# Performance work log

Measured on AMD Instinct MI355X. Metric: run time of the kernel, lower is better.

Reference implementation:

```python
import jax, jax.numpy as jnp
import numpy as np


def setup_inputs() -> dict:
    key = jax.random.key(0)
    kq, kk, kv = jax.random.split(key, 3)
    B, Hq, Hkv, S, D = 2, 16, 4, 2048, 64
    q = jax.random.normal(kq, (B, Hq, S, D), dtype=jnp.float32)
    k = jax.random.normal(kk, (B, Hkv, S, D), dtype=jnp.float32)
    v = jax.random.normal(kv, (B, Hkv, S, D), dtype=jnp.float32)
    return {"q": q, "k": k, "v": v}


def reference(q, k, v):
    # SDPA MATH backend: softmax(q k^T * scale) v, with GQA head repetition.
    Hq = q.shape[1]
    Hkv = k.shape[1]
    rep = Hq // Hkv
    if rep > 1:
        k = jnp.repeat(k, rep, axis=1)  # [B,Hq,S,D]
        v = jnp.repeat(v, rep, axis=1)
    scale = 1.0 / jnp.sqrt(jnp.asarray(q.shape[-1], dtype=q.dtype))
    scores = jnp.einsum("bhqd,bhkd->bhqk", q, k) * scale  # [B,Hq,S,S]
    attn = jax.nn.softmax(scores, axis=-1)
    return jnp.einsum("bhqk,bhkd->bhqd", attn, v)
```

## Files before the change

kernel.cpp:

```cpp
#include <hip/hip_runtime.h>
#include <hip/hip_bf16.h>

typedef unsigned short u16;
typedef short s16x4 __attribute__((ext_vector_type(4)));
typedef short s16x8 __attribute__((ext_vector_type(8)));
typedef float fx4 __attribute__((ext_vector_type(4)));
typedef unsigned ux2 __attribute__((ext_vector_type(2)));

#define BATCH 2
#define NHQ 16
#define NHKV 4
#define SEQ 2048
#define HD 64
#define TM 128
#define TN 128
#define NTILES (SEQ / TN)
#define VSTRIDE 132
#define NKV (BATCH * NHKV * SEQ * HD)
#define QSCALE 0.18033688011112042f

__device__ __forceinline__ unsigned pack2_bf16(float a, float b) {
    const unsigned ua = __float_as_uint(a) + 0x8000u;
    const unsigned ub = __float_as_uint(b) + 0x8000u;
    return __builtin_amdgcn_perm(ub, ua, 0x07060302u);
}
__device__ __forceinline__ unsigned ilv_lo(unsigned r0, unsigned r1) {
    return __builtin_amdgcn_perm(r1, r0, 0x05040100u);
}
__device__ __forceinline__ unsigned ilv_hi(unsigned r0, unsigned r1) {
    return __builtin_amdgcn_perm(r1, r0, 0x07060302u);
}

__global__ __launch_bounds__(256) void cvt_kv_kernel(
    const float* __restrict__ K, const float* __restrict__ V,
    u16* __restrict__ wsK, u16* __restrict__ wsV)
{
    const int i = (blockIdx.x * 256 + threadIdx.x) * 4;
    const fx4 k4 = *(const fx4*)(K + i);
    const fx4 v4 = *(const fx4*)(V + i);
    ux2 ko, vo;
    ko[0] = pack2_bf16(k4[0], k4[1]);
    ko[1] = pack2_bf16(k4[2], k4[3]);
    vo[0] = pack2_bf16(v4[0], v4[1]);
    vo[1] = pack2_bf16(v4[2], v4[3]);
    *(ux2*)(wsK + i) = ko;
    *(ux2*)(wsV + i) = vo;
}

__global__ __launch_bounds__(256, 2) void ptSDPA_39668317946373_kernel(
    const float* __restrict__ gQ,
    const u16* __restrict__ wsK,
    const u16* __restrict__ wsV,
    float* __restrict__ gO)
{
    __shared__ u16 shK[2][TN * HD];
    __shared__ u16 shVt[2][HD * VSTRIDE];

    const int tid = threadIdx.x;
    const int wv  = tid >> 6;
    const int ln  = tid & 63;
    const int l15 = ln & 15;
    const int qd  = ln >> 4;

    const int g     = blockIdx.x;
    const int kvg   = g & 7;
    const int inner = g >> 3;
    const int qtb   = inner & 15;
    const int hqw   = inner >> 4;
    const int batch = kvg >> 2;
    const int hkv   = kvg & 3;
    const int head  = batch * NHQ + hkv * 4 + hqw;

    const int t0 = (inner & 3) * 4;

    const float* q_base = gQ + (size_t)head * SEQ * HD;
    const u16*   k_base = wsK + (size_t)kvg * SEQ * HD;
    const u16*   v_base = wsV + (size_t)kvg * SEQ * HD;
    float*       o_base = gO + (size_t)head * SEQ * HD;

    const int qrow0 = qtb * TM;

    s16x8 qfrag[2][2];
#pragma unroll
    for (int mi = 0; mi < 2; mi++) {
        const int row = qrow0 + wv * 32 + mi * 16 + l15;
#pragma unroll
        for (int ks = 0; ks < 2; ks++) {
            const int d0 = ks * 32 + qd * 8;
            const fx4 lo = *(const fx4*)(q_base + (size_t)row * HD + d0);
            const fx4 hi = *(const fx4*)(q_base + (size_t)row * HD + d0 + 4);
            union { unsigned u[4]; s16x8 v; } t;
            t.u[0] = pack2_bf16(lo[0] * QSCALE, lo[1] * QSCALE);
            t.u[1] = pack2_bf16(lo[2] * QSCALE, lo[3] * QSCALE);
            t.u[2] = pack2_bf16(hi[0] * QSCALE, hi[1] * QSCALE);
            t.u[3] = pack2_bf16(hi[2] * QSCALE, hi[3] * QSCALE);
            qfrag[mi][ks] = t.v;
        }
    }

    fx4 oacc[2][4];
    fx4 racc[2];
    const fx4 z4 = {0.f, 0.f, 0.f, 0.f};
#pragma unroll
    for (int mi = 0; mi < 2; mi++) {
        racc[mi] = z4;
#pragma unroll
        for (int ni = 0; ni < 4; ni++) oacc[mi][ni] = z4;
    }
    const s16x4 ones4 = {(short)0x3F80, (short)0x3F80,
                         (short)0x3F80, (short)0x3F80};

    const int skey  = tid & 127;
    const int shalf = tid >> 7;
    const u16* kp0 = k_base + skey * HD + shalf * 32;
    const int vkey = ln * 2;
    const int vd0  = wv * 16;
    const u16* vp0 = v_base + vkey * HD + vd0;

    s16x8 kreg[4], vreg[4];

#pragma unroll
    for (int s = 0; s < 4; s++)
        kreg[s] = *(const s16x8*)(kp0 + (size_t)t0 * TN * HD + s * 8);
    {
        const u16* vp = vp0 + (size_t)t0 * TN * HD;
        vreg[0] = *(const s16x8*)(vp);
        vreg[1] = *(const s16x8*)(vp + 8);
        vreg[2] = *(const s16x8*)(vp + HD);
        vreg[3] = *(const s16x8*)(vp + HD + 8);
    }
#pragma unroll
    for (int s = 0; s < 4; s++) {
        const int c = shalf * 4 + s;
        *(s16x8*)(shK[0] + skey * 64 + ((c ^ (skey & 7)) * 8)) = kreg[s];
    }
#pragma unroll
    for (int h = 0; h < 2; h++) {
        union { s16x8 v; unsigned u[4]; } r0, r1;
        r0.v = vreg[h];
        r1.v = vreg[2 + h];
#pragma unroll
        for (int c2 = 0; c2 < 4; c2++) {
            const int d = vd0 + h * 8 + c2 * 2;
            *(unsigned*)(shVt[0] + d * VSTRIDE + vkey) = ilv_lo(r0.u[c2], r1.u[c2]);
            *(unsigned*)(shVt[0] + (d + 1) * VSTRIDE + vkey) = ilv_hi(r0.u[c2], r1.u[c2]);
        }
    }

#pragma unroll 2
    for (int i = 0; i < NTILES; i++) {
        const int cur = i & 1;
        const int nxt = cur ^ 1;

        __syncthreads();

        if (i + 1 < NTILES) {
            const int tp = (t0 + i + 1) & (NTILES - 1);
            const u16* kp = kp0 + (size_t)tp * TN * HD;
            const u16* vp = vp0 + (size_t)tp * TN * HD;
#pragma unroll
            for (int s = 0; s < 4; s++) kreg[s] = *(const s16x8*)(kp + s * 8);
            vreg[0] = *(const s16x8*)(vp);
            vreg[1] = *(const s16x8*)(vp + 8);
            vreg[2] = *(const s16x8*)(vp + HD);
            vreg[3] = *(const s16x8*)(vp + HD + 8);
        }

        const int kb7 = l15 & 7;
        const int sw0 = (qd ^ kb7) << 3;
        const int sw1 = ((4 + qd) ^ kb7) << 3;
        const u16* kRow = shK[cur] + l15 * 64;

        fx4 scp[2][2];
        {
            const s16x8 kf0 = *(const s16x8*)(kRow + sw0);
            const s16x8 kf1 = *(const s16x8*)(kRow + sw1);
#pragma unroll
            for (int mi = 0; mi < 2; mi++)
                scp[0][mi] = __builtin_amdgcn_mfma_f32_16x16x32_bf16(
                    kf0, qfrag[mi][0], z4, 0, 0, 0);
#pragma unroll
            for (int mi = 0; mi < 2; mi++)
                scp[0][mi] = __builtin_amdgcn_mfma_f32_16x16x32_bf16(
                    kf1, qfrag[mi][1], scp[0][mi], 0, 0, 0);
        }

#pragma unroll
        for (int kt = 0; kt < 8; kt++) {
            const int p = kt & 1;
            if (kt < 7) {
                const s16x8 kf0 = *(const s16x8*)(kRow + (kt + 1) * 1024 + sw0);
                const s16x8 kf1 = *(const s16x8*)(kRow + (kt + 1) * 1024 + sw1);
#pragma unroll
                for (int mi = 0; mi < 2; mi++)
                    scp[p ^ 1][mi] = __builtin_amdgcn_mfma_f32_16x16x32_bf16(
                        kf0, qfrag[mi][0], z4, 0, 0, 0);
#pragma unroll
                for (int mi = 0; mi < 2; mi++)
                    scp[p ^ 1][mi] = __builtin_amdgcn_mfma_f32_16x16x32_bf16(
                        kf1, qfrag[mi][1], scp[p ^ 1][mi], 0, 0, 0);
            }

            const int kb = kt * 16 + qd * 4;
            s16x4 vf[4];
#pragma unroll
            for (int ni = 0; ni < 4; ni++)
                vf[ni] = *(const s16x4*)(
                    shVt[cur] + (ni * 16 + l15) * VSTRIDE + kb);

            s16x4 pf[2];
#pragma unroll
            for (int mi = 0; mi < 2; mi++) {
                const float p0 = __builtin_amdgcn_exp2f(scp[p][mi][0]);
                const float p1 = __builtin_amdgcn_exp2f(scp[p][mi][1]);
                const float p2 = __builtin_amdgcn_exp2f(scp[p][mi][2]);
                const float p3 = __builtin_amdgcn_exp2f(scp[p][mi][3]);
                union { unsigned u[2]; s16x4 v; } pp;
                pp.u[0] = pack2_bf16(p0, p1);
                pp.u[1] = pack2_bf16(p2, p3);
                pf[mi] = pp.v;
            }

#pragma unroll
            for (int mi = 0; mi < 2; mi++)
                racc[mi] = __builtin_amdgcn_mfma_f32_16x16x16bf16_1k(
                    pf[mi], ones4, racc[mi], 0, 0, 0);

#pragma unroll
            for (int ni = 0; ni < 4; ni++) {
#pragma unroll
                for (int mi = 0; mi < 2; mi++)
                    oacc[mi][ni] = __builtin_amdgcn_mfma_f32_16x16x16bf16_1k(
                        pf[mi], vf[ni], oacc[mi][ni], 0, 0, 0);
            }
        }

        if (i + 1 < NTILES) {
#pragma unroll
            for (int s = 0; s < 4; s++) {
                const int c = shalf * 4 + s;
                *(s16x8*)(shK[nxt] + skey * 64 + ((c ^ (skey & 7)) * 8)) = kreg[s];
            }
#pragma unroll
            for (int h = 0; h < 2; h++) {
                union { s16x8 v; unsigned u[4]; } r0, r1;
                r0.v = vreg[h];
                r1.v = vreg[2 + h];
#pragma unroll
                for (int c2 = 0; c2 < 4; c2++) {
                    const int d = vd0 + h * 8 + c2 * 2;
                    *(unsigned*)(shVt[nxt] + d * VSTRIDE + vkey) =
                        ilv_lo(r0.u[c2], r1.u[c2]);
                    *(unsigned*)(shVt[nxt] + (d + 1) * VSTRIDE + vkey) =
                        ilv_hi(r0.u[c2], r1.u[c2]);
                }
            }
        }
    }

#pragma unroll
    for (int mi = 0; mi < 2; mi++) {
        float inv[4];
#pragma unroll
        for (int r = 0; r < 4; r++) inv[r] = 1.0f / racc[mi][r];
#pragma unroll
        for (int ni = 0; ni < 4; ni++)
#pragma unroll
            for (int r = 0; r < 4; r++) {
                const int qr = qrow0 + wv * 32 + mi * 16 + qd * 4 + r;
                o_base[(size_t)qr * HD + ni * 16 + l15] =
                    oacc[mi][ni][r] * inv[r];
            }
    }
}

extern "C" void kernel_launch(void* const* d_in, const int* in_sizes, int n_in,
                              void* d_out, int out_size, void* d_ws, size_t ws_size,
                              hipStream_t stream) {
    const float* q = (const float*)d_in[0];
    const float* k = (const float*)d_in[1];
    const float* v = (const float*)d_in[2];
    float*       o = (float*)d_out;
    u16* wsK = (u16*)d_ws;
    u16* wsV = wsK + NKV;
    cvt_kv_kernel<<<NKV / 1024, 256, 0, stream>>>(k, v, wsK, wsV);
    const dim3 grid(BATCH * NHQ * (SEQ / TM));
    ptSDPA_39668317946373_kernel<<<grid, 256, 0, stream>>>(q, wsK, wsV, o);
}
```

Baseline: 126.3 us.

## Use 8 waves per block with 16 query rows each and split K/V loading

Doubles the block to 512 threads so each wave owns 16 query rows instead of 32, halving per-wave accumulators and MFMA work per tile. The global-to-LDS staging is split so that half the waves load V (with transpose) and half load K, instead of every thread loading both. The goal is more waves in flight to hide latency, with lower register pressure and less staging work per thread. In exchange each wave does less MFMA work per LDS fragment read, so K/V shared-memory reads per FLOP go up, and there is more barrier overhead across a larger block.

Result: faster. 123.3 us (-2.4%).

```diff
diff --git a/kernel.cpp b/kernel.cpp
--- a/kernel.cpp
+++ b/kernel.cpp
@@ -47,7 +47,7 @@
     *(ux2*)(wsV + i) = vo;
 }
 
-__global__ __launch_bounds__(256, 2) void ptSDPA_39668317946373_kernel(
+__global__ __launch_bounds__(512, 4) void ptSDPA_39668317946373_kernel(
     const float* __restrict__ gQ,
     const u16* __restrict__ wsK,
     const u16* __restrict__ wsV,
@@ -80,10 +80,9 @@
 
     const int qrow0 = qtb * TM;
 
-    s16x8 qfrag[2][2];
-#pragma unroll
-    for (int mi = 0; mi < 2; mi++) {
-        const int row = qrow0 + wv * 32 + mi * 16 + l15;
+    s16x8 qfrag[2];
+    {
+        const int row = qrow0 + wv * 16 + l15;
 #pragma unroll
         for (int ks = 0; ks < 2; ks++) {
             const int d0 = ks * 32 + qd * 8;
@@ -94,56 +93,58 @@
             t.u[1] = pack2_bf16(lo[2] * QSCALE, lo[3] * QSCALE);
             t.u[2] = pack2_bf16(hi[0] * QSCALE, hi[1] * QSCALE);
             t.u[3] = pack2_bf16(hi[2] * QSCALE, hi[3] * QSCALE);
-            qfrag[mi][ks] = t.v;
-        }
-    }
-
-    fx4 oacc[2][4];
-    fx4 racc[2];
+            qfrag[ks] = t.v;
+        }
+    }
+
+    fx4 oacc[4];
+    fx4 racc;
     const fx4 z4 = {0.f, 0.f, 0.f, 0.f};
-#pragma unroll
-    for (int mi = 0; mi < 2; mi++) {
-        racc[mi] = z4;
-#pragma unroll
-        for (int ni = 0; ni < 4; ni++) oacc[mi][ni] = z4;
-    }
+    racc = z4;
+#pragma unroll
+    for (int ni = 0; ni < 4; ni++) oacc[ni] = z4;
     const s16x4 ones4 = {(short)0x3F80, (short)0x3F80,
                          (short)0x3F80, (short)0x3F80};
 
-    const int skey  = tid & 127;
-    const int shalf = tid >> 7;
+    const bool isV = (wv < 4);
+    const int  st  = isV ? tid : (tid - 256);
+    const int vkey = (st & 63) * 2;
+    const int vd0  = (st >> 6) * 16;
+    const u16* vp0 = v_base + vkey * HD + vd0;
+    const int skey  = st & 127;
+    const int shalf = st >> 7;
     const u16* kp0 = k_base + skey * HD + shalf * 32;
-    const int vkey = ln * 2;
-    const int vd0  = wv * 16;
-    const u16* vp0 = v_base + vkey * HD + vd0;
-
-    s16x8 kreg[4], vreg[4];
-
-#pragma unroll
-    for (int s = 0; s < 4; s++)
-        kreg[s] = *(const s16x8*)(kp0 + (size_t)t0 * TN * HD + s * 8);
-    {
+
+    s16x8 preg[4];
+
+    if (isV) {
         const u16* vp = vp0 + (size_t)t0 * TN * HD;
-        vreg[0] = *(const s16x8*)(vp);
-        vreg[1] = *(const s16x8*)(vp + 8);
-        vreg[2] = *(const s16x8*)(vp + HD);
-        vreg[3] = *(const s16x8*)(vp + HD + 8);
-    }
-#pragma unroll
-    for (int s = 0; s < 4; s++) {
-        const int c = shalf * 4 + s;
-        *(s16x8*)(shK[0] + skey * 64 + ((c ^ (skey & 7)) * 8)) = kreg[s];
-    }
-#pragma unroll
-    for (int h = 0; h < 2; h++) {
-        union { s16x8 v; unsigned u[4]; } r0, r1;
-        r0.v = vreg[h];
-        r1.v = vreg[2 + h];
-#pragma unroll
-        for (int c2 = 0; c2 < 4; c2++) {
-            const int d = vd0 + h * 8 + c2 * 2;
-            *(unsigned*)(shVt[0] + d * VSTRIDE + vkey) = ilv_lo(r0.u[c2], r1.u[c2]);
-            *(unsigned*)(shVt[0] + (d + 1) * VSTRIDE + vkey) = ilv_hi(r0.u[c2], r1.u[c2]);
+        preg[0] = *(const s16x8*)(vp);
+        preg[1] = *(const s16x8*)(vp + 8);
+        preg[2] = *(const s16x8*)(vp + HD);
+        preg[3] = *(const s16x8*)(vp + HD + 8);
+#pragma unroll
+        for (int h = 0; h < 2; h++) {
+            union { s16x8 v; unsigned u[4]; } r0, r1;
+            r0.v = preg[h];
+            r1.v = preg[2 + h];
+#pragma unroll
+            for (int c2 = 0; c2 < 4; c2++) {
+                const int d = vd0 + h * 8 + c2 * 2;
+                *(unsigned*)(shVt[0] + d * VSTRIDE + vkey) =
+                    ilv_lo(r0.u[c2], r1.u[c2]);
+                *(unsigned*)(shVt[0] + (d + 1) * VSTRIDE + vkey) =
+                    ilv_hi(r0.u[c2], r1.u[c2]);
+            }
+        }
+    } else {
+#pragma unroll
+        for (int s = 0; s < 4; s++)
+            preg[s] = *(const s16x8*)(kp0 + (size_t)t0 * TN * HD + s * 8);
+#pragma unroll
+        for (int s = 0; s < 4; s++) {
+            const int c = shalf * 4 + s;
+            *(s16x8*)(shK[0] + skey * 64 + ((c ^ (skey & 7)) * 8)) = preg[s];
         }
     }
 
@@ -156,14 +157,18 @@
 
         if (i + 1 < NTILES) {
             const int tp = (t0 + i + 1) & (NTILES - 1);
-            const u16* kp = kp0 + (size_t)tp * TN * HD;
-            const u16* vp = vp0 + (size_t)tp * TN * HD;
-#pragma unroll
-            for (int s = 0; s < 4; s++) kreg[s] = *(const s16x8*)(kp + s * 8);
-            vreg[0] = *(const s16x8*)(vp);
-            vreg[1] = *(const s16x8*)(vp + 8);
-            vreg[2] = *(const s16x8*)(vp + HD);
-            vreg[3] = *(const s16x8*)(vp + HD + 8);
+            if (isV) {
+                const u16* vp = vp0 + (size_t)tp * TN * HD;
+                preg[0] = *(const s16x8*)(vp);
+                preg[1] = *(const s16x8*)(vp + 8);
+                preg[2] = *(const s16x8*)(vp + HD);
+                preg[3] = *(const s16x8*)(vp + HD + 8);
+            } else {
+                const u16* kp = kp0 + (size_t)tp * TN * HD;
+#pragma unroll
+                for (int s = 0; s < 4; s++)
+                    preg[s] = *(const s16x8*)(kp + s * 8);
+            }
         }
 
         const int kb7 = l15 & 7;
@@ -171,18 +176,14 @@
         const int sw1 = ((4 + qd) ^ kb7) << 3;
         const u16* kRow = shK[cur] + l15 * 64;
 
-        fx4 scp[2][2];
+        fx4 scp[2];
         {
             const s16x8 kf0 = *(const s16x8*)(kRow + sw0);
             const s16x8 kf1 = *(const s16x8*)(kRow + sw1);
-#pragma unroll
-            for (int mi = 0; mi < 2; mi++)
-                scp[0][mi] = __builtin_amdgcn_mfma_f32_16x16x32_bf16(
-                    kf0, qfrag[mi][0], z4, 0, 0, 0);
-#pragma unroll
-            for (int mi = 0; mi < 2; mi++)
-                scp[0][mi] = __builtin_amdgcn_mfma_f32_16x16x32_bf16(
-                    kf1, qfrag[mi][1], scp[0][mi], 0, 0, 0);
+            scp[0] = __builtin_amdgcn_mfma_f32_16x16x32_bf16(
+                kf0, qfrag[0], z4, 0, 0, 0);
+            scp[0] = __builtin_amdgcn_mfma_f32_16x16x32_bf16(
+                kf1, qfrag[1], scp[0], 0, 0, 0);
         }
 
 #pragma unroll
@@ -191,14 +192,10 @@
             if (kt < 7) {
                 const s16x8 kf0 = *(const s16x8*)(kRow + (kt + 1) * 1024 + sw0);
                 const s16x8 kf1 = *(const s16x8*)(kRow + (kt + 1) * 1024 + sw1);
-#pragma unroll
-                for (int mi = 0; mi < 2; mi++)
-                    scp[p ^ 1][mi] = __builtin_amdgcn_mfma_f32_16x16x32_bf16(
-                        kf0, qfrag[mi][0], z4, 0, 0, 0);
-#pragma unroll
-                for (int mi = 0; mi < 2; mi++)
-                    scp[p ^ 1][mi] = __builtin_amdgcn_mfma_f32_16x16x32_bf16(
-                        kf1, qfrag[mi][1], scp[p ^ 1][mi], 0, 0, 0);
+                scp[p ^ 1] = __builtin_amdgcn_mfma_f32_16x16x32_bf16(
+                    kf0, qfrag[0], z4, 0, 0, 0);
+                scp[p ^ 1] = __builtin_amdgcn_mfma_f32_16x16x32_bf16(
+                    kf1, qfrag[1], scp[p ^ 1], 0, 0, 0);
             }
 
             const int kb = kt * 16 + qd * 4;
@@ -208,68 +205,62 @@
                 vf[ni] = *(const s16x4*)(
                     shVt[cur] + (ni * 16 + l15) * VSTRIDE + kb);
 
-            s16x4 pf[2];
-#pragma unroll
-            for (int mi = 0; mi < 2; mi++) {
-                const float p0 = __builtin_amdgcn_exp2f(scp[p][mi][0]);
-                const float p1 = __builtin_amdgcn_exp2f(scp[p][mi][1]);
-                const float p2 = __builtin_amdgcn_exp2f(scp[p][mi][2]);
-                const float p3 = __builtin_amdgcn_exp2f(scp[p][mi][3]);
-                union { unsigned u[2]; s16x4 v; } pp;
-                pp.u[0] = pack2_bf16(p0, p1);
-                pp.u[1] = pack2_bf16(p2, p3);
-                pf[mi] = pp.v;
-            }
-
-#pragma unroll
-            for (int mi = 0; mi < 2; mi++)
-                racc[mi] = __builtin_amdgcn_mfma_f32_16x16x16bf16_1k(
-                    pf[mi], ones4, racc[mi], 0, 0, 0);
-
-#pragma unroll
-            for (int ni = 0; ni < 4; ni++) {
-#pragma unroll
-                for (int mi = 0; mi < 2; mi++)
-                    oacc[mi][ni] = __builtin_amdgcn_mfma_f32_16x16x16bf16_1k(
-                        pf[mi], vf[ni], oacc[mi][ni], 0, 0, 0);
-            }
+            const float p0 = __builtin_amdgcn_exp2f(scp[p][0]);
+            const float p1 = __builtin_amdgcn_exp2f(scp[p][1]);
+            const float p2 = __builtin_amdgcn_exp2f(scp[p][2]);
+            const float p3 = __builtin_amdgcn_exp2f(scp[p][3]);
+            union { unsigned u[2]; s16x4 v; } pp;
+            pp.u[0] = pack2_bf16(p0, p1);
+            pp.u[1] = pack2_bf16(p2, p3);
+            const s16x4 pf = pp.v;
+
+            racc = __builtin_amdgcn_mfma_f32_16x16x16bf16_1k(
+                pf, ones4, racc, 0, 0, 0);
+
+#pragma unroll
+            for (int ni = 0; ni < 4; ni++)
+                oacc[ni] = __builtin_amdgcn_mfma_f32_16x16x16bf16_1k(
+                    pf, vf[ni], oacc[ni], 0, 0, 0);
         }
 
         if (i + 1 < NTILES) {
-#pragma unroll
-            for (int s = 0; s < 4; s++) {
-                const int c = shalf * 4 + s;
-                *(s16x8*)(shK[nxt] + skey * 64 + ((c ^ (skey & 7)) * 8)) = kreg[s];
-            }
-#pragma unroll
-            for (int h = 0; h < 2; h++) {
-                union { s16x8 v; unsigned u[4]; } r0, r1;
-                r0.v = vreg[h];
-                r1.v = vreg[2 + h];
-#pragma unroll
-                for (int c2 = 0; c2 < 4; c2++) {
-                    const int d = vd0 + h * 8 + c2 * 2;
-                    *(unsigned*)(shVt[nxt] + d * VSTRIDE + vkey) =
-                        ilv_lo(r0.u[c2], r1.u[c2]);
-                    *(unsigned*)(shVt[nxt] + (d + 1) * VSTRIDE + vkey) =
-                        ilv_hi(r0.u[c2], r1.u[c2]);
+            if (isV) {
+#pragma unroll
+                for (int h = 0; h < 2; h++) {
+                    union { s16x8 v; unsigned u[4]; } r0, r1;
+                    r0.v = preg[h];
+                    r1.v = preg[2 + h];
+#pragma unroll
+                    for (int c2 = 0; c2 < 4; c2++) {
+                        const int d = vd0 + h * 8 + c2 * 2;
+                        *(unsigned*)(shVt[nxt] + d * VSTRIDE + vkey) =
+                            ilv_lo(r0.u[c2], r1.u[c2]);
+                        *(unsigned*)(shVt[nxt] + (d + 1) * VSTRIDE + vkey) =
+                            ilv_hi(r0.u[c2], r1.u[c2]);
+                    }
                 }
-            }
-        }
-    }
-
-#pragma unroll
-    for (int mi = 0; mi < 2; mi++) {
+            } else {
+#pragma unroll
+                for (int s = 0; s < 4; s++) {
+                    const int c = shalf * 4 + s;
+                    *(s16x8*)(shK[nxt] + skey * 64 + ((c ^ (skey & 7)) * 8)) =
+                        preg[s];
+                }
+            }
+        }
+    }
+
+    {
         float inv[4];
 #pragma unroll
-        for (int r = 0; r < 4; r++) inv[r] = 1.0f / racc[mi][r];
+        for (int r = 0; r < 4; r++) inv[r] = 1.0f / racc[r];
 #pragma unroll
         for (int ni = 0; ni < 4; ni++)
 #pragma unroll
             for (int r = 0; r < 4; r++) {
-                const int qr = qrow0 + wv * 32 + mi * 16 + qd * 4 + r;
+                const int qr = qrow0 + wv * 16 + qd * 4 + r;
                 o_base[(size_t)qr * HD + ni * 16 + l15] =
-                    oacc[mi][ni][r] * inv[r];
+                    oacc[ni][r] * inv[r];
             }
     }
 }
@@ -285,5 +276,5 @@
     u16* wsV = wsK + NKV;
     cvt_kv_kernel<<<NKV / 1024, 256, 0, stream>>>(k, v, wsK, wsV);
     const dim3 grid(BATCH * NHQ * (SEQ / TM));
-    ptSDPA_39668317946373_kernel<<<grid, 256, 0, stream>>>(q, wsK, wsV, o);
-}
+    ptSDPA_39668317946373_kernel<<<grid, 512, 0, stream>>>(q, wsK, wsV, o);
+}
```

## Split key tile across two wave groups with 512-thread blocks and LDS reduction

Applied to the files above, without the earlier changes.

Doubles the block to 512 threads. Each group of four waves handles half of the 128-key tile for the same 32 query rows, and the two groups' partial output and row-sum accumulators are combined through shared memory at the end. Tile loading is split so the first 256 threads stage V and the other 256 stage K, which halves each thread's prefetch registers. The aim is more waves per CU and more latency hiding. The cost is an extra reduction pass through LDS with two more barriers, and 512-thread blocks that must fit four per CU under the tighter register limit.

Measured after the change: 135.9 us. 7.6% more time.

```diff
diff --git a/kernel.cpp b/kernel.cpp
--- a/kernel.cpp
+++ b/kernel.cpp
@@ -47,7 +47,7 @@
     *(ux2*)(wsV + i) = vo;
 }
 
-__global__ __launch_bounds__(256, 2) void ptSDPA_39668317946373_kernel(
+__global__ __launch_bounds__(512, 4) void ptSDPA_39668317946373_kernel(
     const float* __restrict__ gQ,
     const u16* __restrict__ wsK,
     const u16* __restrict__ wsV,
@@ -58,6 +58,8 @@
 
     const int tid = threadIdx.x;
     const int wv  = tid >> 6;
+    const int qw  = wv & 3;
+    const int kh  = wv >> 2;
     const int ln  = tid & 63;
     const int l15 = ln & 15;
     const int qd  = ln >> 4;
@@ -83,7 +85,7 @@
     s16x8 qfrag[2][2];
 #pragma unroll
     for (int mi = 0; mi < 2; mi++) {
-        const int row = qrow0 + wv * 32 + mi * 16 + l15;
+        const int row = qrow0 + qw * 32 + mi * 16 + l15;
 #pragma unroll
         for (int ks = 0; ks < 2; ks++) {
             const int d0 = ks * 32 + qd * 8;
@@ -110,42 +112,49 @@
     const s16x4 ones4 = {(short)0x3F80, (short)0x3F80,
                          (short)0x3F80, (short)0x3F80};
 
-    const int skey  = tid & 127;
-    const int shalf = tid >> 7;
+    const bool isV = (wv < 4);
+    const int  st  = isV ? tid : (tid - 256);
+    const int vkey = (st & 63) * 2;
+    const int vd0  = (st >> 6) * 16;
+    const u16* vp0 = v_base + vkey * HD + vd0;
+    const int skey  = st & 127;
+    const int shalf = st >> 7;
     const u16* kp0 = k_base + skey * HD + shalf * 32;
-    const int vkey = ln * 2;
-    const int vd0  = wv * 16;
-    const u16* vp0 = v_base + vkey * HD + vd0;
-
-    s16x8 kreg[4], vreg[4];
-
-#pragma unroll
-    for (int s = 0; s < 4; s++)
-        kreg[s] = *(const s16x8*)(kp0 + (size_t)t0 * TN * HD + s * 8);
-    {
+
+    s16x8 preg[4];
+
+    if (isV) {
         const u16* vp = vp0 + (size_t)t0 * TN * HD;
-        vreg[0] = *(const s16x8*)(vp);
-        vreg[1] = *(const s16x8*)(vp + 8);
-        vreg[2] = *(const s16x8*)(vp + HD);
-        vreg[3] = *(const s16x8*)(vp + HD + 8);
-    }
-#pragma unroll
-    for (int s = 0; s < 4; s++) {
-        const int c = shalf * 4 + s;
-        *(s16x8*)(shK[0] + skey * 64 + ((c ^ (skey & 7)) * 8)) = kreg[s];
-    }
-#pragma unroll
-    for (int h = 0; h < 2; h++) {
-        union { s16x8 v; unsigned u[4]; } r0, r1;
-        r0.v = vreg[h];
-        r1.v = vreg[2 + h];
-#pragma unroll
-        for (int c2 = 0; c2 < 4; c2++) {
-            const int d = vd0 + h * 8 + c2 * 2;
-            *(unsigned*)(shVt[0] + d * VSTRIDE + vkey) = ilv_lo(r0.u[c2], r1.u[c2]);
-            *(unsigned*)(shVt[0] + (d + 1) * VSTRIDE + vkey) = ilv_hi(r0.u[c2], r1.u[c2]);
-        }
-    }
+        preg[0] = *(const s16x8*)(vp);
+        preg[1] = *(const s16x8*)(vp + 8);
+        preg[2] = *(const s16x8*)(vp + HD);
+        preg[3] = *(const s16x8*)(vp + HD + 8);
+#pragma unroll
+        for (int h = 0; h < 2; h++) {
+            union { s16x8 v; unsigned u[4]; } r0, r1;
+            r0.v = preg[h];
+            r1.v = preg[2 + h];
+#pragma unroll
+            for (int c2 = 0; c2 < 4; c2++) {
+                const int d = vd0 + h * 8 + c2 * 2;
+                *(unsigned*)(shVt[0] + d * VSTRIDE + vkey) =
+                    ilv_lo(r0.u[c2], r1.u[c2]);
+                *(unsigned*)(shVt[0] + (d + 1) * VSTRIDE + vkey) =
+                    ilv_hi(r0.u[c2], r1.u[c2]);
+            }
+        }
+    } else {
+#pragma unroll
+        for (int s = 0; s < 4; s++)
+            preg[s] = *(const s16x8*)(kp0 + (size_t)t0 * TN * HD + s * 8);
+#pragma unroll
+        for (int s = 0; s < 4; s++) {
+            const int c = shalf * 4 + s;
+            *(s16x8*)(shK[0] + skey * 64 + ((c ^ (skey & 7)) * 8)) = preg[s];
+        }
+    }
+
+    const int ktbase = kh * 4;
 
 #pragma unroll 2
     for (int i = 0; i < NTILES; i++) {
@@ -156,14 +165,18 @@
 
         if (i + 1 < NTILES) {
             const int tp = (t0 + i + 1) & (NTILES - 1);
-            const u16* kp = kp0 + (size_t)tp * TN * HD;
-            const u16* vp = vp0 + (size_t)tp * TN * HD;
-#pragma unroll
-            for (int s = 0; s < 4; s++) kreg[s] = *(const s16x8*)(kp + s * 8);
-            vreg[0] = *(const s16x8*)(vp);
-            vreg[1] = *(const s16x8*)(vp + 8);
-            vreg[2] = *(const s16x8*)(vp + HD);
-            vreg[3] = *(const s16x8*)(vp + HD + 8);
+            if (isV) {
+                const u16* vp = vp0 + (size_t)tp * TN * HD;
+                preg[0] = *(const s16x8*)(vp);
+                preg[1] = *(const s16x8*)(vp + 8);
+                preg[2] = *(const s16x8*)(vp + HD);
+                preg[3] = *(const s16x8*)(vp + HD + 8);
+            } else {
+                const u16* kp = kp0 + (size_t)tp * TN * HD;
+#pragma unroll
+                for (int s = 0; s < 4; s++)
+                    preg[s] = *(const s16x8*)(kp + s * 8);
+            }
         }
 
         const int kb7 = l15 & 7;
@@ -173,8 +186,8 @@
 
         fx4 scp[2][2];
         {
-            const s16x8 kf0 = *(const s16x8*)(kRow + sw0);
-            const s16x8 kf1 = *(const s16x8*)(kRow + sw1);
+            const s16x8 kf0 = *(const s16x8*)(kRow + ktbase * 1024 + sw0);
+            const s16x8 kf1 = *(const s16x8*)(kRow + ktbase * 1024 + sw1);
 #pragma unroll
             for (int mi = 0; mi < 2; mi++)
                 scp[0][mi] = __builtin_amdgcn_mfma_f32_16x16x32_bf16(
@@ -186,11 +199,13 @@
         }
 
 #pragma unroll
-        for (int kt = 0; kt < 8; kt++) {
+        for (int kt = 0; kt < 4; kt++) {
             const int p = kt & 1;
-            if (kt < 7) {
-                const s16x8 kf0 = *(const s16x8*)(kRow + (kt + 1) * 1024 + sw0);
-                const s16x8 kf1 = *(const s16x8*)(kRow + (kt + 1) * 1024 + sw1);
+            if (kt < 3) {
+                const s16x8 kf0 =
+                    *(const s16x8*)(kRow + (ktbase + kt + 1) * 1024 + sw0);
+                const s16x8 kf1 =
+                    *(const s16x8*)(kRow + (ktbase + kt + 1) * 1024 + sw1);
 #pragma unroll
                 for (int mi = 0; mi < 2; mi++)
                     scp[p ^ 1][mi] = __builtin_amdgcn_mfma_f32_16x16x32_bf16(
@@ -201,7 +216,7 @@
                         kf1, qfrag[mi][1], scp[p ^ 1][mi], 0, 0, 0);
             }
 
-            const int kb = kt * 16 + qd * 4;
+            const int kb = (ktbase + kt) * 16 + qd * 4;
             s16x4 vf[4];
 #pragma unroll
             for (int ni = 0; ni < 4; ni++)
@@ -236,41 +251,77 @@
         }
 
         if (i + 1 < NTILES) {
-#pragma unroll
-            for (int s = 0; s < 4; s++) {
-                const int c = shalf * 4 + s;
-                *(s16x8*)(shK[nxt] + skey * 64 + ((c ^ (skey & 7)) * 8)) = kreg[s];
-            }
-#pragma unroll
-            for (int h = 0; h < 2; h++) {
-                union { s16x8 v; unsigned u[4]; } r0, r1;
-                r0.v = vreg[h];
-                r1.v = vreg[2 + h];
-#pragma unroll
-                for (int c2 = 0; c2 < 4; c2++) {
-                    const int d = vd0 + h * 8 + c2 * 2;
-                    *(unsigned*)(shVt[nxt] + d * VSTRIDE + vkey) =
-                        ilv_lo(r0.u[c2], r1.u[c2]);
-                    *(unsigned*)(shVt[nxt] + (d + 1) * VSTRIDE + vkey) =
-                        ilv_hi(r0.u[c2], r1.u[c2]);
+            if (isV) {
+#pragma unroll
+                for (int h = 0; h < 2; h++) {
+                    union { s16x8 v; unsigned u[4]; } r0, r1;
+                    r0.v = preg[h];
+                    r1.v = preg[2 + h];
+#pragma unroll
+                    for (int c2 = 0; c2 < 4; c2++) {
+                        const int d = vd0 + h * 8 + c2 * 2;
+                        *(unsigned*)(shVt[nxt] + d * VSTRIDE + vkey) =
+                            ilv_lo(r0.u[c2], r1.u[c2]);
+                        *(unsigned*)(shVt[nxt] + (d + 1) * VSTRIDE + vkey) =
+                            ilv_hi(r0.u[c2], r1.u[c2]);
+                    }
                 }
-            }
-        }
-    }
-
-#pragma unroll
-    for (int mi = 0; mi < 2; mi++) {
-        float inv[4];
-#pragma unroll
-        for (int r = 0; r < 4; r++) inv[r] = 1.0f / racc[mi][r];
-#pragma unroll
-        for (int ni = 0; ni < 4; ni++)
-#pragma unroll
-            for (int r = 0; r < 4; r++) {
-                const int qr = qrow0 + wv * 32 + mi * 16 + qd * 4 + r;
-                o_base[(size_t)qr * HD + ni * 16 + l15] =
-                    oacc[mi][ni][r] * inv[r];
-            }
+            } else {
+#pragma unroll
+                for (int s = 0; s < 4; s++) {
+                    const int c = shalf * 4 + s;
+                    *(s16x8*)(shK[nxt] + skey * 64 + ((c ^ (skey & 7)) * 8)) =
+                        preg[s];
+                }
+            }
+        }
+    }
+
+    __syncthreads();
+    float* mo = (float*)&shK[0][0];
+    float* mr = (float*)&shVt[0][0];
+    if (kh == 1) {
+        const int slot = qw * 64 + ln;
+#pragma unroll
+        for (int mi = 0; mi < 2; mi++) {
+#pragma unroll
+            for (int ni = 0; ni < 4; ni++)
+#pragma unroll
+                for (int r = 0; r < 4; r++)
+                    mo[((mi * 4 + ni) * 4 + r) * 256 + slot] = oacc[mi][ni][r];
+#pragma unroll
+            for (int r = 0; r < 4; r++)
+                mr[(mi * 4 + r) * 256 + slot] = racc[mi][r];
+        }
+    }
+    __syncthreads();
+    if (kh == 0) {
+        const int slot = qw * 64 + ln;
+#pragma unroll
+        for (int mi = 0; mi < 2; mi++) {
+#pragma unroll
+            for (int ni = 0; ni < 4; ni++)
+#pragma unroll
+                for (int r = 0; r < 4; r++)
+                    oacc[mi][ni][r] += mo[((mi * 4 + ni) * 4 + r) * 256 + slot];
+#pragma unroll
+            for (int r = 0; r < 4; r++)
+                racc[mi][r] += mr[(mi * 4 + r) * 256 + slot];
+        }
+#pragma unroll
+        for (int mi = 0; mi < 2; mi++) {
+            float inv[4];
+#pragma unroll
+            for (int r = 0; r < 4; r++) inv[r] = 1.0f / racc[mi][r];
+#pragma unroll
+            for (int ni = 0; ni < 4; ni++)
+#pragma unroll
+                for (int r = 0; r < 4; r++) {
+                    const int qr = qrow0 + qw * 32 + mi * 16 + qd * 4 + r;
+                    o_base[(size_t)qr * HD + ni * 16 + l15] =
+                        oacc[mi][ni][r] * inv[r];
+                }
+        }
     }
 }
 
@@ -285,5 +336,5 @@
     u16* wsV = wsK + NKV;
     cvt_kv_kernel<<<NKV / 1024, 256, 0, stream>>>(k, v, wsK, wsV);
     const dim3 grid(BATCH * NHQ * (SEQ / TM));
-    ptSDPA_39668317946373_kernel<<<grid, 256, 0, stream>>>(q, wsK, wsV, o);
-}
+    ptSDPA_39668317946373_kernel<<<grid, 512, 0, stream>>>(q, wsK, wsV, o);
+}
```

## Warp-specialize attention kernel into compute and K/V loader waves

Applied to the files above, without the earlier changes.

Doubles the block to 512 threads. Four waves do only the QK/PV MFMA compute, and four dedicated producer waves load the next K/V tile from global memory and write it into the double-buffered LDS. The goal is to take global load latency and LDS stores off the compute waves' critical path. In exchange, producer waves hold scheduler slots without doing math, and launch_bounds(512,4) asks for 16 waves per CU, which may squeeze registers and spill the compute accumulators. Nothing runs unmasked on the `!isC` side after the loop. The same barrier per tile is kept.

Measured after the change: 120.0 us. -5.0%, faster.

```diff
diff --git a/kernel.cpp b/kernel.cpp
--- a/kernel.cpp
+++ b/kernel.cpp
@@ -47,7 +47,7 @@
     *(ux2*)(wsV + i) = vo;
 }
 
-__global__ __launch_bounds__(256, 2) void ptSDPA_39668317946373_kernel(
+__global__ __launch_bounds__(512, 4) void ptSDPA_39668317946373_kernel(
     const float* __restrict__ gQ,
     const u16* __restrict__ wsK,
     const u16* __restrict__ wsV,
@@ -80,24 +80,9 @@
 
     const int qrow0 = qtb * TM;
 
+    const bool isC = (wv < 4);
+
     s16x8 qfrag[2][2];
-#pragma unroll
-    for (int mi = 0; mi < 2; mi++) {
-        const int row = qrow0 + wv * 32 + mi * 16 + l15;
-#pragma unroll
-        for (int ks = 0; ks < 2; ks++) {
-            const int d0 = ks * 32 + qd * 8;
-            const fx4 lo = *(const fx4*)(q_base + (size_t)row * HD + d0);
-            const fx4 hi = *(const fx4*)(q_base + (size_t)row * HD + d0 + 4);
-            union { unsigned u[4]; s16x8 v; } t;
-            t.u[0] = pack2_bf16(lo[0] * QSCALE, lo[1] * QSCALE);
-            t.u[1] = pack2_bf16(lo[2] * QSCALE, lo[3] * QSCALE);
-            t.u[2] = pack2_bf16(hi[0] * QSCALE, hi[1] * QSCALE);
-            t.u[3] = pack2_bf16(hi[2] * QSCALE, hi[3] * QSCALE);
-            qfrag[mi][ks] = t.v;
-        }
-    }
-
     fx4 oacc[2][4];
     fx4 racc[2];
     const fx4 z4 = {0.f, 0.f, 0.f, 0.f};
@@ -110,40 +95,61 @@
     const s16x4 ones4 = {(short)0x3F80, (short)0x3F80,
                          (short)0x3F80, (short)0x3F80};
 
-    const int skey  = tid & 127;
-    const int shalf = tid >> 7;
+    if (isC) {
+#pragma unroll
+        for (int mi = 0; mi < 2; mi++) {
+            const int row = qrow0 + wv * 32 + mi * 16 + l15;
+#pragma unroll
+            for (int ks = 0; ks < 2; ks++) {
+                const int d0 = ks * 32 + qd * 8;
+                const fx4 lo = *(const fx4*)(q_base + (size_t)row * HD + d0);
+                const fx4 hi = *(const fx4*)(q_base + (size_t)row * HD + d0 + 4);
+                union { unsigned u[4]; s16x8 v; } t;
+                t.u[0] = pack2_bf16(lo[0] * QSCALE, lo[1] * QSCALE);
+                t.u[1] = pack2_bf16(lo[2] * QSCALE, lo[3] * QSCALE);
+                t.u[2] = pack2_bf16(hi[0] * QSCALE, hi[1] * QSCALE);
+                t.u[3] = pack2_bf16(hi[2] * QSCALE, hi[3] * QSCALE);
+                qfrag[mi][ks] = t.v;
+            }
+        }
+    }
+
+    const int st = tid - 256;
+    const int skey  = st & 127;
+    const int shalf = st >> 7;
     const u16* kp0 = k_base + skey * HD + shalf * 32;
-    const int vkey = ln * 2;
-    const int vd0  = wv * 16;
+    const int vkey = (st & 63) * 2;
+    const int vd0  = (st >> 6) * 16;
     const u16* vp0 = v_base + vkey * HD + vd0;
 
-    s16x8 kreg[4], vreg[4];
-
-#pragma unroll
-    for (int s = 0; s < 4; s++)
-        kreg[s] = *(const s16x8*)(kp0 + (size_t)t0 * TN * HD + s * 8);
-    {
+    if (!isC) {
+        s16x8 kreg[4], vreg[4];
+        const u16* kp = kp0 + (size_t)t0 * TN * HD;
         const u16* vp = vp0 + (size_t)t0 * TN * HD;
+#pragma unroll
+        for (int s = 0; s < 4; s++) kreg[s] = *(const s16x8*)(kp + s * 8);
         vreg[0] = *(const s16x8*)(vp);
         vreg[1] = *(const s16x8*)(vp + 8);
         vreg[2] = *(const s16x8*)(vp + HD);
         vreg[3] = *(const s16x8*)(vp + HD + 8);
-    }
-#pragma unroll
-    for (int s = 0; s < 4; s++) {
-        const int c = shalf * 4 + s;
-        *(s16x8*)(shK[0] + skey * 64 + ((c ^ (skey & 7)) * 8)) = kreg[s];
-    }
-#pragma unroll
-    for (int h = 0; h < 2; h++) {
-        union { s16x8 v; unsigned u[4]; } r0, r1;
-        r0.v = vreg[h];
-        r1.v = vreg[2 + h];
-#pragma unroll
-        for (int c2 = 0; c2 < 4; c2++) {
-            const int d = vd0 + h * 8 + c2 * 2;
-            *(unsigned*)(shVt[0] + d * VSTRIDE + vkey) = ilv_lo(r0.u[c2], r1.u[c2]);
-            *(unsigned*)(shVt[0] + (d + 1) * VSTRIDE + vkey) = ilv_hi(r0.u[c2], r1.u[c2]);
+#pragma unroll
+        for (int s = 0; s < 4; s++) {
+            const int c = shalf * 4 + s;
+            *(s16x8*)(shK[0] + skey * 64 + ((c ^ (skey & 7)) * 8)) = kreg[s];
+        }
+#pragma unroll
+        for (int h = 0; h < 2; h++) {
+            union { s16x8 v; unsigned u[4]; } r0, r1;
+            r0.v = vreg[h];
+            r1.v = vreg[2 + h];
+#pragma unroll
+            for (int c2 = 0; c2 < 4; c2++) {
+                const int d = vd0 + h * 8 + c2 * 2;
+                *(unsigned*)(shVt[0] + d * VSTRIDE + vkey) =
+                    ilv_lo(r0.u[c2], r1.u[c2]);
+                *(unsigned*)(shVt[0] + (d + 1) * VSTRIDE + vkey) =
+                    ilv_hi(r0.u[c2], r1.u[c2]);
+            }
         }
     }
 
@@ -154,123 +160,132 @@
 
         __syncthreads();
 
-        if (i + 1 < NTILES) {
-            const int tp = (t0 + i + 1) & (NTILES - 1);
-            const u16* kp = kp0 + (size_t)tp * TN * HD;
-            const u16* vp = vp0 + (size_t)tp * TN * HD;
-#pragma unroll
-            for (int s = 0; s < 4; s++) kreg[s] = *(const s16x8*)(kp + s * 8);
-            vreg[0] = *(const s16x8*)(vp);
-            vreg[1] = *(const s16x8*)(vp + 8);
-            vreg[2] = *(const s16x8*)(vp + HD);
-            vreg[3] = *(const s16x8*)(vp + HD + 8);
-        }
-
-        const int kb7 = l15 & 7;
-        const int sw0 = (qd ^ kb7) << 3;
-        const int sw1 = ((4 + qd) ^ kb7) << 3;
-        const u16* kRow = shK[cur] + l15 * 64;
-
-        fx4 scp[2][2];
-        {
-            const s16x8 kf0 = *(const s16x8*)(kRow + sw0);
-            const s16x8 kf1 = *(const s16x8*)(kRow + sw1);
-#pragma unroll
-            for (int mi = 0; mi < 2; mi++)
-                scp[0][mi] = __builtin_amdgcn_mfma_f32_16x16x32_bf16(
-                    kf0, qfrag[mi][0], z4, 0, 0, 0);
-#pragma unroll
-            for (int mi = 0; mi < 2; mi++)
-                scp[0][mi] = __builtin_amdgcn_mfma_f32_16x16x32_bf16(
-                    kf1, qfrag[mi][1], scp[0][mi], 0, 0, 0);
-        }
-
-#pragma unroll
-        for (int kt = 0; kt < 8; kt++) {
-            const int p = kt & 1;
-            if (kt < 7) {
-                const s16x8 kf0 = *(const s16x8*)(kRow + (kt + 1) * 1024 + sw0);
-                const s16x8 kf1 = *(const s16x8*)(kRow + (kt + 1) * 1024 + sw1);
+        if (isC) {
+            const int kb7 = l15 & 7;
+            const int sw0 = (qd ^ kb7) << 3;
+            const int sw1 = ((4 + qd) ^ kb7) << 3;
+            const u16* kRow = shK[cur] + l15 * 64;
+
+            fx4 scp[2][2];
+            {
+                const s16x8 kf0 = *(const s16x8*)(kRow + sw0);
+                const s16x8 kf1 = *(const s16x8*)(kRow + sw1);
 #pragma unroll
                 for (int mi = 0; mi < 2; mi++)
-                    scp[p ^ 1][mi] = __builtin_amdgcn_mfma_f32_16x16x32_bf16(
+                    scp[0][mi] = __builtin_amdgcn_mfma_f32_16x16x32_bf16(
                         kf0, qfrag[mi][0], z4, 0, 0, 0);
 #pragma unroll
                 for (int mi = 0; mi < 2; mi++)
-                    scp[p ^ 1][mi] = __builtin_amdgcn_mfma_f32_16x16x32_bf16(
-                        kf1, qfrag[mi][1], scp[p ^ 1][mi], 0, 0, 0);
-            }
-
-            const int kb = kt * 16 + qd * 4;
-            s16x4 vf[4];
+                    scp[0][mi] = __builtin_amdgcn_mfma_f32_16x16x32_bf16(
+                        kf1, qfrag[mi][1], scp[0][mi], 0, 0, 0);
+            }
+
+#pragma unroll
+            for (int kt = 0; kt < 8; kt++) {
+                const int p = kt & 1;
+                if (kt < 7) {
+                    const s16x8 kf0 =
+                        *(const s16x8*)(kRow + (kt + 1) * 1024 + sw0);
+                    const s16x8 kf1 =
+                        *(const s16x8*)(kRow + (kt + 1) * 1024 + sw1);
+#pragma unroll
+                    for (int mi = 0; mi < 2; mi++)
+                        scp[p ^ 1][mi] =
+                            __builtin_amdgcn_mfma_f32_16x16x32_bf16(
+                                kf0, qfrag[mi][0], z4, 0, 0, 0);
+#pragma unroll
+                    for (int mi = 0; mi < 2; mi++)
+                        scp[p ^ 1][mi] =
+                            __builtin_amdgcn_mfma_f32_16x16x32_bf16(
+                                kf1, qfrag[mi][1], scp[p ^ 1][mi], 0, 0, 0);
+                }
+
+                const int kb = kt * 16 + qd * 4;
+                s16x4 vf[4];
+#pragma unroll
+                for (int ni = 0; ni < 4; ni++)
+                    vf[ni] = *(const s16x4*)(
+                        shVt[cur] + (ni * 16 + l15) * VSTRIDE + kb);
+
+                s16x4 pf[2];
+#pragma unroll
+                for (int mi = 0; mi < 2; mi++) {
+                    const float p0 = __builtin_amdgcn_exp2f(scp[p][mi][0]);
+                    const float p1 = __builtin_amdgcn_exp2f(scp[p][mi][1]);
+                    const float p2 = __builtin_amdgcn_exp2f(scp[p][mi][2]);
+                    const float p3 = __builtin_amdgcn_exp2f(scp[p][mi][3]);
+                    union { unsigned u[2]; s16x4 v; } pp;
+                    pp.u[0] = pack2_bf16(p0, p1);
+                    pp.u[1] = pack2_bf16(p2, p3);
+                    pf[mi] = pp.v;
+                }
+
+#pragma unroll
+                for (int mi = 0; mi < 2; mi++)
+                    racc[mi] = __builtin_amdgcn_mfma_f32_16x16x16bf16_1k(
+                        pf[mi], ones4, racc[mi], 0, 0, 0);
+
+#pragma unroll
+                for (int ni = 0; ni < 4; ni++) {
+#pragma unroll
+                    for (int mi = 0; mi < 2; mi++)
+                        oacc[mi][ni] =
+                            __builtin_amdgcn_mfma_f32_16x16x16bf16_1k(
+                                pf[mi], vf[ni], oacc[mi][ni], 0, 0, 0);
+                }
+            }
+        } else {
+            if (i + 1 < NTILES) {
+                const int tp = (t0 + i + 1) & (NTILES - 1);
+                s16x8 kreg[4], vreg[4];
+                const u16* kp = kp0 + (size_t)tp * TN * HD;
+                const u16* vp = vp0 + (size_t)tp * TN * HD;
+#pragma unroll
+                for (int s = 0; s < 4; s++)
+                    kreg[s] = *(const s16x8*)(kp + s * 8);
+                vreg[0] = *(const s16x8*)(vp);
+                vreg[1] = *(const s16x8*)(vp + 8);
+                vreg[2] = *(const s16x8*)(vp + HD);
+                vreg[3] = *(const s16x8*)(vp + HD + 8);
+#pragma unroll
+                for (int s = 0; s < 4; s++) {
+                    const int c = shalf * 4 + s;
+                    *(s16x8*)(shK[nxt] + skey * 64 + ((c ^ (skey & 7)) * 8)) =
+                        kreg[s];
+                }
+#pragma unroll
+                for (int h = 0; h < 2; h++) {
+                    union { s16x8 v; unsigned u[4]; } r0, r1;
+                    r0.v = vreg[h];
+                    r1.v = vreg[2 + h];
+#pragma unroll
+                    for (int c2 = 0; c2 < 4; c2++) {
+                        const int d = vd0 + h * 8 + c2 * 2;
+                        *(unsigned*)(shVt[nxt] + d * VSTRIDE + vkey) =
+                            ilv_lo(r0.u[c2], r1.u[c2]);
+                        *(unsigned*)(shVt[nxt] + (d + 1) * VSTRIDE + vkey) =
+                            ilv_hi(r0.u[c2], r1.u[c2]);
+                    }
+                }
+            }
+        }
+    }
+
+    if (isC) {
+#pragma unroll
+        for (int mi = 0; mi < 2; mi++) {
+            float inv[4];
+#pragma unroll
+            for (int r = 0; r < 4; r++) inv[r] = 1.0f / racc[mi][r];
 #pragma unroll
             for (int ni = 0; ni < 4; ni++)
-                vf[ni] = *(const s16x4*)(
-                    shVt[cur] + (ni * 16 + l15) * VSTRIDE + kb);
-
-            s16x4 pf[2];
-#pragma unroll
-            for (int mi = 0; mi < 2; mi++) {
-                const float p0 = __builtin_amdgcn_exp2f(scp[p][mi][0]);
-                const float p1 = __builtin_amdgcn_exp2f(scp[p][mi][1]);
-                const float p2 = __builtin_amdgcn_exp2f(scp[p][mi][2]);
-                const float p3 = __builtin_amdgcn_exp2f(scp[p][mi][3]);
-                union { unsigned u[2]; s16x4 v; } pp;
-                pp.u[0] = pack2_bf16(p0, p1);
-                pp.u[1] = pack2_bf16(p2, p3);
-                pf[mi] = pp.v;
-            }
-
-#pragma unroll
-            for (int mi = 0; mi < 2; mi++)
-                racc[mi] = __builtin_amdgcn_mfma_f32_16x16x16bf16_1k(
-                    pf[mi], ones4, racc[mi], 0, 0, 0);
-
-#pragma unroll
-            for (int ni = 0; ni < 4; ni++) {
-#pragma unroll
-                for (int mi = 0; mi < 2; mi++)
-                    oacc[mi][ni] = __builtin_amdgcn_mfma_f32_16x16x16bf16_1k(
-                        pf[mi], vf[ni], oacc[mi][ni], 0, 0, 0);
-            }
-        }
-
-        if (i + 1 < NTILES) {
-#pragma unroll
-            for (int s = 0; s < 4; s++) {
-                const int c = shalf * 4 + s;
-                *(s16x8*)(shK[nxt] + skey * 64 + ((c ^ (skey & 7)) * 8)) = kreg[s];
-            }
-#pragma unroll
-            for (int h = 0; h < 2; h++) {
-                union { s16x8 v; unsigned u[4]; } r0, r1;
-                r0.v = vreg[h];
-                r1.v = vreg[2 + h];
-#pragma unroll
-                for (int c2 = 0; c2 < 4; c2++) {
-                    const int d = vd0 + h * 8 + c2 * 2;
-                    *(unsigned*)(shVt[nxt] + d * VSTRIDE + vkey) =
-                        ilv_lo(r0.u[c2], r1.u[c2]);
-                    *(unsigned*)(shVt[nxt] + (d + 1) * VSTRIDE + vkey) =
-                        ilv_hi(r0.u[c2], r1.u[c2]);
-                }
-            }
-        }
-    }
-
-#pragma unroll
-    for (int mi = 0; mi < 2; mi++) {
-        float inv[4];
-#pragma unroll
-        for (int r = 0; r < 4; r++) inv[r] = 1.0f / racc[mi][r];
-#pragma unroll
-        for (int ni = 0; ni < 4; ni++)
-#pragma unroll
-            for (int r = 0; r < 4; r++) {
-                const int qr = qrow0 + wv * 32 + mi * 16 + qd * 4 + r;
-                o_base[(size_t)qr * HD + ni * 16 + l15] =
-                    oacc[mi][ni][r] * inv[r];
-            }
+#pragma unroll
+                for (int r = 0; r < 4; r++) {
+                    const int qr = qrow0 + wv * 32 + mi * 16 + qd * 4 + r;
+                    o_base[(size_t)qr * HD + ni * 16 + l15] =
+                        oacc[mi][ni][r] * inv[r];
+                }
+        }
     }
 }
 
@@ -285,5 +300,5 @@
     u16* wsV = wsK + NKV;
     cvt_kv_kernel<<<NKV / 1024, 256, 0, stream>>>(k, v, wsK, wsV);
     const dim3 grid(BATCH * NHQ * (SEQ / TM));
-    ptSDPA_39668317946373_kernel<<<grid, 256, 0, stream>>>(q, wsK, wsV, o);
-}
+    ptSDPA_39668317946373_kernel<<<grid, 512, 0, stream>>>(q, wsK, wsV, o);
+}
```
